# Performance work log

Measured on AMD Instinct MI355X. Metric: run time of the kernel, lower is better.

## Reference

```python
import jax, jax.numpy as jnp
import numpy as np

N_QUBITS = 12
FAST_DEPTH = 4
FAST_DECAY = 0.9
LATENT = 512
BATCH = 2048


def _apply_ry(state, theta, wire):
    # state: (B, 2**n) real; RY is a real rotation. PennyLane default.qubit:
    # wire 0 is the most-significant bit of the state index.
    B = state.shape[0]
    s = state.reshape(B, 1 << wire, 2, -1)
    h = theta * 0.5
    c = jnp.cos(h)[:, None, None]
    sn = jnp.sin(h)[:, None, None]
    s0, s1 = s[:, :, 0], s[:, :, 1]
    out = jnp.stack([c * s0 - sn * s1, sn * s0 + c * s1], axis=2)
    return out.reshape(state.shape)


def _apply_cnot_adjacent(state, wire):
    # CNOT with control=wire, target=wire+1 (nearest-neighbor chain)
    B = state.shape[0]
    s = state.reshape(B, 1 << wire, 2, 2, -1)
    out = jnp.stack([s[:, :, 0], s[:, :, 1, ::-1]], axis=2)
    return out.reshape(state.shape)


def _fwp_circuit(x, fast, n_qubits, n_outputs):
    # x: (B, n_qubits) RY encoding angles; fast: (B, depth, n_qubits)
    B = x.shape[0]
    dim = 1 << n_qubits
    # Hadamard layer on |0...0> -> uniform positive real amplitudes.
    state = jnp.full((B, dim), 2.0 ** (-n_qubits / 2), dtype=x.dtype)
    for w in range(n_qubits):
        state = _apply_ry(state, x[:, w], w)
    for layer in range(fast.shape[1]):
        for w in range(n_qubits - 1):
            state = _apply_cnot_adjacent(state, w)
        for w in range(n_qubits):
            state = _apply_ry(state, fast[:, layer, w], w)
    probs = state * state  # real state -> |amp|^2
    outs = []
    for w in range(n_outputs):
        p = probs.reshape(B, 1 << w, 2, -1)
        outs.append(p[:, :, 0].sum(axis=(1, 2)) - p[:, :, 1].sum(axis=(1, 2)))
    return jnp.stack(outs, axis=1)  # (B, n_outputs) PauliZ expvals


def setup_inputs() -> dict:
    key = jax.random.key(0)
    ks = jax.random.split(key, 6)
    n, depth, latent = N_QUBITS, FAST_DEPTH, LATENT
    return {
        "x_t": jax.random.normal(ks[0], (BATCH, n), jnp.float32),
        "fast_prev": jax.random.normal(ks[1], (BATCH, depth, n), jnp.float32) * 0.1,
        "W_enc": jax.random.normal(ks[2], (latent, n), jnp.float32) / np.sqrt(n).astype(np.float32),
        "b_enc": jnp.zeros((latent,), jnp.float32),
        "W_upd": jax.random.normal(ks[3], (depth * n, latent), jnp.float32) / np.sqrt(latent).astype(np.float32),
        "b_upd": jnp.zeros((depth * n,), jnp.float32),
        "W_ro": jax.random.normal(ks[4], (1, n), jnp.float32) / np.sqrt(n).astype(np.float32),
        "b_ro": jnp.zeros((1,), jnp.float32),
    }


def reference(x_t, fast_prev, W_enc, b_enc, W_upd, b_upd, W_ro, b_ro):
    latent = jnp.tanh(x_t @ W_enc.T + b_enc)
    delta = (latent @ W_upd.T + b_upd).reshape(x_t.shape[0], FAST_DEPTH, N_QUBITS)
    fast_next = FAST_DECAY * fast_prev + delta
    q_out = _fwp_circuit(x_t, fast_next, N_QUBITS, N_QUBITS)  # n_outputs = n_qubits
    y_t = q_out @ W_ro.T + b_ro
    return (y_t, fast_next)
```

## Files before the change

### kernel.cpp

```cpp
#include <hip/hip_runtime.h>

static constexpr int NQ    = 12;
static constexpr int DEPTH = 4;
static constexpr int LAT   = 512;
static constexpr int FAST  = DEPTH * NQ;
static constexpr float DECAY = 0.9f;
static constexpr int P     = 68;

using v2f = __attribute__((ext_vector_type(2))) float;


__device__ __forceinline__ constexpr int G6(int x)  { return (x ^ (x >> 1)) & 63; }
__device__ __forceinline__ constexpr int GINV(int x){ int y = x; y ^= y >> 1; y ^= y >> 2; y ^= y >> 4; return y & 63; }

template<int CTRL>
__device__ __forceinline__ float dppf(float x){
    return __int_as_float(__builtin_amdgcn_mov_dpp(__float_as_int(x), CTRL, 0xF, 0xF, false));
}
template<int B> __device__ __forceinline__ float lexch(float x);
template<> __device__ __forceinline__ float lexch<0>(float x){ return dppf<0xB1>(x); }
template<> __device__ __forceinline__ float lexch<1>(float x){ return dppf<0x4E>(x); }
template<> __device__ __forceinline__ float lexch<2>(float x){ return dppf<0x141>(dppf<0x1B>(x)); }
template<> __device__ __forceinline__ float lexch<3>(float x){ return dppf<0x128>(x); }
template<> __device__ __forceinline__ float lexch<4>(float x){
    return __int_as_float(__builtin_amdgcn_ds_swizzle(__float_as_int(x), 0x401F));
}

template<int B>
__device__ __forceinline__ void lanewire(float (&t)[64], float c, float ss){
    #pragma unroll
    for (int k = 0; k < 64; k++){
        float p = lexch<B>(t[k]);
        t[k] = __builtin_fmaf(c, t[k], ss * p);
    }
}

template<int B>
__device__ __forceinline__ void regwire(float (&t)[64], float c, float s){
    constexpr int M = (B == 0) ? 1 : ((1 << B) | (1 << (B - 1)));
    #pragma unroll
    for (int k = 0; k < 64; k++){
        if (__builtin_parity((unsigned)(k >> B)) == 0){
            float a = t[k], b = t[k ^ M];
            t[k]     = c * a - s * b;
            t[k ^ M] = s * a + c * b;
        }
    }
}

__device__ __forceinline__ void stageW(const float (&t)[64], float* X, int wbase){
    #pragma unroll
    for (int m = 0; m < 16; m++)
        *(float4*)&X[wbase + 4*m] =
            (float4){ t[G6(4*m+0)], t[G6(4*m+1)], t[G6(4*m+2)], t[G6(4*m+3)] };
}

__device__ __forceinline__ void stageR0(float (&t)[64], const float* X, int rs, int rp, int off,
                                        float c0, float ss0){
    #pragma unroll
    for (int m = 0; m < 16; m++){
        int col = (4*m) ^ off;
        float4 a = *(const float4*)&X[rs + col];
        float4 b = *(const float4*)&X[rp + col];
        t[4*m+0] = __builtin_fmaf(c0, a.x, ss0 * b.x);
        t[4*m+1] = __builtin_fmaf(c0, a.y, ss0 * b.y);
        t[4*m+2] = __builtin_fmaf(c0, a.z, ss0 * b.z);
        t[4*m+3] = __builtin_fmaf(c0, a.w, ss0 * b.w);
    }
}

__device__ __forceinline__ void wiresLane(float (&t)[64], const v2f* c, int lane){
    { v2f cs = c[1]; lanewire<4>(t, cs.x, (lane & 16) ? cs.y : -cs.y); }
    { v2f cs = c[2]; lanewire<3>(t, cs.x, (lane &  8) ? cs.y : -cs.y); }
    { v2f cs = c[3]; lanewire<2>(t, cs.x, (lane &  4) ? cs.y : -cs.y); }
    { v2f cs = c[4]; lanewire<1>(t, cs.x, (lane &  2) ? cs.y : -cs.y); }
    { v2f cs = c[5]; lanewire<0>(t, cs.x, (lane &  1) ? cs.y : -cs.y); }
}
__device__ __forceinline__ void wiresReg(float (&t)[64], const v2f* c){
    { v2f cs = c[6];  regwire<5>(t, cs.x, cs.y); }
    { v2f cs = c[7];  regwire<4>(t, cs.x, cs.y); }
    { v2f cs = c[8];  regwire<3>(t, cs.x, cs.y); }
    { v2f cs = c[9];  regwire<2>(t, cs.x, cs.y); }
    { v2f cs = c[10]; regwire<1>(t, cs.x, cs.y); }
    { v2f cs = c[11]; regwire<0>(t, cs.x, cs.y); }
}

__device__ __forceinline__ void init_state(float (&v)[64], const float (&xa)[NQ], int lane) {
    float g0[NQ], g1[NQ];
    #pragma unroll
    for (int w = 0; w < NQ; w++) {
        float hh = 0.5f * xa[w];
        float c = __cosf(hh), s = __sinf(hh);
        g0[w] = (c - s) * 0.70710678118654752f;
        g1[w] = (c + s) * 0.70710678118654752f;
    }
    float L = 1.0f;
    #pragma unroll
    for (int w = 0; w < 6; w++)
        L *= ((lane >> (5 - w)) & 1) ? g1[w] : g0[w];
    v[0] = L;
    #pragma unroll
    for (int w = 6; w < NQ; w++) {
        const int S = 1 << (11 - w);
        #pragma unroll
        for (int r = 0; r < 64; r += 2 * S) {
            v[r + S] = v[r] * g1[w];
            v[r]     = v[r] * g0[w];
        }
    }
}

__global__ __launch_bounds__(64, 1)
void fwp_kernel(const float* __restrict__ x_t,
                const float* __restrict__ fast_prev,
                const float* __restrict__ W_enc,
                const float* __restrict__ b_enc,
                const float* __restrict__ W_upd,
                const float* __restrict__ b_upd,
                const float* __restrict__ W_ro,
                const float* __restrict__ b_ro,
                float* __restrict__ out_y,
                float* __restrict__ out_fast) {
    const int lane = threadIdx.x;
    const int eA   = 2 * blockIdx.x;
    const int eB   = eA + 1;

    __shared__ __align__(16) float XA[64 * P];
    __shared__ __align__(16) float XB[64 * P];
    __shared__ __align__(8)  v2f   csA[FAST], csB[FAST];

    float* latA = XA;
    float* latB = XB;

    float xaA[NQ], xaB[NQ];
    #pragma unroll
    for (int k = 0; k < NQ; k++) {
        xaA[k] = x_t[eA * NQ + k];
        xaB[k] = x_t[eB * NQ + k];
    }

    {
        const float4* we = (const float4*)(W_enc + lane * 8 * NQ);
        float4 be0 = *(const float4*)&b_enc[8 * lane];
        float4 be1 = *(const float4*)&b_enc[8 * lane + 4];
        float be[8] = {be0.x, be0.y, be0.z, be0.w, be1.x, be1.y, be1.z, be1.w};
        float lA[8], lB[8];
        #pragma unroll
        for (int t = 0; t < 8; t++) {
            float4 a0 = we[3 * t], a1 = we[3 * t + 1], a2 = we[3 * t + 2];
            float sA = be[t]
                + a0.x * xaA[0] + a0.y * xaA[1] + a0.z * xaA[2]  + a0.w * xaA[3]
                + a1.x * xaA[4] + a1.y * xaA[5] + a1.z * xaA[6]  + a1.w * xaA[7]
                + a2.x * xaA[8] + a2.y * xaA[9] + a2.z * xaA[10] + a2.w * xaA[11];
            float sB = be[t]
                + a0.x * xaB[0] + a0.y * xaB[1] + a0.z * xaB[2]  + a0.w * xaB[3]
                + a1.x * xaB[4] + a1.y * xaB[5] + a1.z * xaB[6]  + a1.w * xaB[7]
                + a2.x * xaB[8] + a2.y * xaB[9] + a2.z * xaB[10] + a2.w * xaB[11];
            lA[t] = tanhf(sA);
            lB[t] = tanhf(sB);
        }
        *(float4*)&latA[8 * lane]     = (float4){lA[0], lA[1], lA[2], lA[3]};
        *(float4*)&latA[8 * lane + 4] = (float4){lA[4], lA[5], lA[6], lA[7]};
        *(float4*)&latB[8 * lane]     = (float4){lB[0], lB[1], lB[2], lB[3]};
        *(float4*)&latB[8 * lane + 4] = (float4){lB[4], lB[5], lB[6], lB[7]};
    }

    if (lane < FAST) {
        const float4* wr = (const float4*)(W_upd + lane * LAT);
        const float4* la = (const float4*)(latA);
        const float4* lb = (const float4*)(latB);
        float base = b_upd[lane];
        float sA = base, sB = base;
        #pragma unroll 8
        for (int j = 0; j < LAT / 4; j++) {
            float4 w4 = wr[j];
            float4 a4 = la[j];
            float4 b4 = lb[j];
            sA += w4.x * a4.x + w4.y * a4.y + w4.z * a4.z + w4.w * a4.w;
            sB += w4.x * b4.x + w4.y * b4.y + w4.z * b4.z + w4.w * b4.w;
        }
        float angA = DECAY * fast_prev[eA * FAST + lane] + sA;
        float angB = DECAY * fast_prev[eB * FAST + lane] + sB;
        out_fast[eA * FAST + lane] = angA;
        out_fast[eB * FAST + lane] = angB;
        csA[lane] = (v2f){__cosf(0.5f * angA), __sinf(0.5f * angA)};
        csB[lane] = (v2f){__cosf(0.5f * angB), __sinf(0.5f * angB)};
    }

    float tmp[64], tA[64], tB[64];
    init_state(tmp, xaA, lane);
    #pragma unroll
    for (int k = 0; k < 64; k++) tA[k] = tmp[GINV(k)];
    init_state(tmp, xaB, lane);
    #pragma unroll
    for (int k = 0; k < 64; k++) tB[k] = tmp[GINV(k)];

    const int wbase = lane * P;
    const int gl    = (lane ^ (lane >> 1)) & 63;
    const int rs    = gl * P;
    const int rp    = (gl ^ 48) * P;
    const int off   = (lane & 1) * 32;

    #pragma unroll 1
    for (int layer = 0; layer < DEPTH; layer++) {
        const v2f* cA = csA + layer * NQ;
        const v2f* cB = csB + layer * NQ;
        v2f a0 = cA[0], b0 = cB[0];
        float ssA0 = (lane & 32) ? a0.y : -a0.y;
        float ssB0 = (lane & 32) ? b0.y : -b0.y;

        stageW(tA, XA, wbase);
        stageR0(tA, XA, rs, rp, off, a0.x, ssA0);
        stageW(tB, XB, wbase);
        wiresLane(tA, cA, lane);
        stageR0(tB, XB, rs, rp, off, b0.x, ssB0);
        wiresReg(tA, cA);
        wiresLane(tB, cB, lane);
        wiresReg(tB, cB);
    }

    float wro[NQ];
    #pragma unroll
    for (int w = 0; w < NQ; w++) wro[w] = W_ro[w];
    float sl = 0.0f;
    #pragma unroll
    for (int w = 0; w < 6; w++)
        sl += ((lane >> (5 - w)) & 1) ? -wro[w] : wro[w];

    float totA = 0.0f, pwA[6] = {0,0,0,0,0,0};
    float totB = 0.0f, pwB[6] = {0,0,0,0,0,0};
    #pragma unroll
    for (int r = 0; r < 64; r++) {
        float aA = tA[G6(r)], aB = tB[G6(r)];
        float pA = aA * aA;
        float pB = aB * aB;
        totA += pA;  totB += pB;
        pwA[0] += (r & 32) ? -pA : pA;  pwB[0] += (r & 32) ? -pB : pB;
        pwA[1] += (r & 16) ? -pA : pA;  pwB[1] += (r & 16) ? -pB : pB;
        pwA[2] += (r & 8)  ? -pA : pA;  pwB[2] += (r & 8)  ? -pB : pB;
        pwA[3] += (r & 4)  ? -pA : pA;  pwB[3] += (r & 4)  ? -pB : pB;
        pwA[4] += (r & 2)  ? -pA : pA;  pwB[4] += (r & 2)  ? -pB : pB;
        pwA[5] += (r & 1)  ? -pA : pA;  pwB[5] += (r & 1)  ? -pB : pB;
    }
    float yA = sl * totA, yB = sl * totB;
    #pragma unroll
    for (int k = 0; k < 6; k++) {
        yA += wro[6 + k] * pwA[k];
        yB += wro[6 + k] * pwB[k];
    }
    #pragma unroll
    for (int m = 32; m >= 1; m >>= 1) {
        yA += __shfl_xor(yA, m, 64);
        yB += __shfl_xor(yB, m, 64);
    }
    if (lane == 0) {
        float br = b_ro[0];
        out_y[eA] = yA + br;
        out_y[eB] = yB + br;
    }
}

extern "C" void kernel_launch(void* const* d_in, const int* in_sizes, int n_in,
                              void* d_out, int out_size, void* d_ws, size_t ws_size,
                              hipStream_t stream) {
    const float* x_t       = (const float*)d_in[0];
    const float* fast_prev = (const float*)d_in[1];
    const float* W_enc     = (const float*)d_in[2];
    const float* b_enc     = (const float*)d_in[3];
    const float* W_upd     = (const float*)d_in[4];
    const float* b_upd     = (const float*)d_in[5];
    const float* W_ro      = (const float*)d_in[6];
    const float* b_ro      = (const float*)d_in[7];
    float* out = (float*)d_out;

    fwp_kernel<<<1024, 64, 0, stream>>>(x_t, fast_prev, W_enc, b_enc,
                                        W_upd, b_upd, W_ro, b_ro,
                                        out , out + 2048 );
}
```

Baseline: 121.6 us.

## Interleave both batch elements into packed v2f state to use packed FP32 math

Stores the two batch elements' amplitudes interleaved as float2 pairs so rotations run as packed v2f multiply/FMA operations that can map to packed FP32 instructions. The register-pair wires now use plain bit indices instead of a Gray-code-permuted layout, and the shared-memory transpose is merged into one wider buffer with a new permuted read pattern. Cos/sin tables are repacked as paired CC/SS arrays. The trade-off is that lane exchanges still need two DPP moves per pair, and register pressure or bank conflicts may change with the wider rows.

```diff
diff --git a/kernel.cpp b/kernel.cpp
--- a/kernel.cpp
+++ b/kernel.cpp
@@ -5,13 +5,12 @@
 static constexpr int LAT   = 512;
 static constexpr int FAST  = DEPTH * NQ;
 static constexpr float DECAY = 0.9f;
-static constexpr int P     = 68;
+static constexpr int PPF   = 132;
 
 using v2f = __attribute__((ext_vector_type(2))) float;
 
 
 __device__ __forceinline__ constexpr int G6(int x)  { return (x ^ (x >> 1)) & 63; }
-__device__ __forceinline__ constexpr int GINV(int x){ int y = x; y ^= y >> 1; y ^= y >> 2; y ^= y >> 4; return y & 63; }
 
 template<int CTRL>
 __device__ __forceinline__ float dppf(float x){
@@ -25,87 +24,28 @@
 template<> __device__ __forceinline__ float lexch<4>(float x){
     return __int_as_float(__builtin_amdgcn_ds_swizzle(__float_as_int(x), 0x401F));
 }
+template<int B> __device__ __forceinline__ v2f lexch2(v2f v){
+    return (v2f){ lexch<B>(v.x), lexch<B>(v.y) };
+}
 
 template<int B>
-__device__ __forceinline__ void lanewire(float (&t)[64], float c, float ss){
+__device__ __forceinline__ void lanewire2(v2f (&u)[64], v2f cc, v2f ssv){
     #pragma unroll
     for (int k = 0; k < 64; k++){
-        float p = lexch<B>(t[k]);
-        t[k] = __builtin_fmaf(c, t[k], ss * p);
-    }
-}
-
-template<int B>
-__device__ __forceinline__ void regwire(float (&t)[64], float c, float s){
-    constexpr int M = (B == 0) ? 1 : ((1 << B) | (1 << (B - 1)));
-    #pragma unroll
-    for (int k = 0; k < 64; k++){
-        if (__builtin_parity((unsigned)(k >> B)) == 0){
-            float a = t[k], b = t[k ^ M];
-            t[k]     = c * a - s * b;
-            t[k ^ M] = s * a + c * b;
-        }
-    }
-}
-
-__device__ __forceinline__ void stageW(const float (&t)[64], float* X, int wbase){
-    #pragma unroll
-    for (int m = 0; m < 16; m++)
-        *(float4*)&X[wbase + 4*m] =
-            (float4){ t[G6(4*m+0)], t[G6(4*m+1)], t[G6(4*m+2)], t[G6(4*m+3)] };
-}
-
-__device__ __forceinline__ void stageR0(float (&t)[64], const float* X, int rs, int rp, int off,
-                                        float c0, float ss0){
-    #pragma unroll
-    for (int m = 0; m < 16; m++){
-        int col = (4*m) ^ off;
-        float4 a = *(const float4*)&X[rs + col];
-        float4 b = *(const float4*)&X[rp + col];
-        t[4*m+0] = __builtin_fmaf(c0, a.x, ss0 * b.x);
-        t[4*m+1] = __builtin_fmaf(c0, a.y, ss0 * b.y);
-        t[4*m+2] = __builtin_fmaf(c0, a.z, ss0 * b.z);
-        t[4*m+3] = __builtin_fmaf(c0, a.w, ss0 * b.w);
-    }
-}
-
-__device__ __forceinline__ void wiresLane(float (&t)[64], const v2f* c, int lane){
-    { v2f cs = c[1]; lanewire<4>(t, cs.x, (lane & 16) ? cs.y : -cs.y); }
-    { v2f cs = c[2]; lanewire<3>(t, cs.x, (lane &  8) ? cs.y : -cs.y); }
-    { v2f cs = c[3]; lanewire<2>(t, cs.x, (lane &  4) ? cs.y : -cs.y); }
-    { v2f cs = c[4]; lanewire<1>(t, cs.x, (lane &  2) ? cs.y : -cs.y); }
-    { v2f cs = c[5]; lanewire<0>(t, cs.x, (lane &  1) ? cs.y : -cs.y); }
-}
-__device__ __forceinline__ void wiresReg(float (&t)[64], const v2f* c){
-    { v2f cs = c[6];  regwire<5>(t, cs.x, cs.y); }
-    { v2f cs = c[7];  regwire<4>(t, cs.x, cs.y); }
-    { v2f cs = c[8];  regwire<3>(t, cs.x, cs.y); }
-    { v2f cs = c[9];  regwire<2>(t, cs.x, cs.y); }
-    { v2f cs = c[10]; regwire<1>(t, cs.x, cs.y); }
-    { v2f cs = c[11]; regwire<0>(t, cs.x, cs.y); }
-}
-
-__device__ __forceinline__ void init_state(float (&v)[64], const float (&xa)[NQ], int lane) {
-    float g0[NQ], g1[NQ];
-    #pragma unroll
-    for (int w = 0; w < NQ; w++) {
-        float hh = 0.5f * xa[w];
-        float c = __cosf(hh), s = __sinf(hh);
-        g0[w] = (c - s) * 0.70710678118654752f;
-        g1[w] = (c + s) * 0.70710678118654752f;
-    }
-    float L = 1.0f;
-    #pragma unroll
-    for (int w = 0; w < 6; w++)
-        L *= ((lane >> (5 - w)) & 1) ? g1[w] : g0[w];
-    v[0] = L;
-    #pragma unroll
-    for (int w = 6; w < NQ; w++) {
-        const int S = 1 << (11 - w);
-        #pragma unroll
-        for (int r = 0; r < 64; r += 2 * S) {
-            v[r + S] = v[r] * g1[w];
-            v[r]     = v[r] * g0[w];
+        v2f p = lexch2<B>(u[k]);
+        u[k] = cc * u[k] + ssv * p;
+    }
+}
+
+template<int BIT>
+__device__ __forceinline__ void regwire2(v2f (&u)[64], v2f cc, v2f ss){
+    constexpr int M = 1 << BIT;
+    #pragma unroll
+    for (int r = 0; r < 64; r++){
+        if (!(r & M)){
+            v2f a = u[r], b = u[r ^ M];
+            u[r]     = cc * a - ss * b;
+            u[r ^ M] = ss * a + cc * b;
         }
     }
 }
@@ -125,12 +65,11 @@
     const int eA   = 2 * blockIdx.x;
     const int eB   = eA + 1;
 
-    __shared__ __align__(16) float XA[64 * P];
-    __shared__ __align__(16) float XB[64 * P];
-    __shared__ __align__(8)  v2f   csA[FAST], csB[FAST];
-
-    float* latA = XA;
-    float* latB = XB;
+    __shared__ __align__(16) float Xs[64 * PPF];
+    __shared__ __align__(8)  v2f CC[FAST], SS[FAST];
+
+    float* latA = Xs;
+    float* latB = Xs + LAT;
 
     float xaA[NQ], xaB[NQ];
     #pragma unroll
@@ -183,40 +122,93 @@
         float angB = DECAY * fast_prev[eB * FAST + lane] + sB;
         out_fast[eA * FAST + lane] = angA;
         out_fast[eB * FAST + lane] = angB;
-        csA[lane] = (v2f){__cosf(0.5f * angA), __sinf(0.5f * angA)};
-        csB[lane] = (v2f){__cosf(0.5f * angB), __sinf(0.5f * angB)};
-    }
-
-    float tmp[64], tA[64], tB[64];
-    init_state(tmp, xaA, lane);
-    #pragma unroll
-    for (int k = 0; k < 64; k++) tA[k] = tmp[GINV(k)];
-    init_state(tmp, xaB, lane);
-    #pragma unroll
-    for (int k = 0; k < 64; k++) tB[k] = tmp[GINV(k)];
-
-    const int wbase = lane * P;
-    const int gl    = (lane ^ (lane >> 1)) & 63;
-    const int rs    = gl * P;
-    const int rp    = (gl ^ 48) * P;
-    const int off   = (lane & 1) * 32;
+        CC[lane] = (v2f){__cosf(0.5f * angA), __cosf(0.5f * angB)};
+        SS[lane] = (v2f){__sinf(0.5f * angA), __sinf(0.5f * angB)};
+    }
+
+    v2f u[64];
+    {
+        v2f g0[NQ], g1[NQ];
+        #pragma unroll
+        for (int w = 0; w < NQ; w++) {
+            float hA = 0.5f * xaA[w], hB = 0.5f * xaB[w];
+            float cA = __cosf(hA), sA = __sinf(hA);
+            float cB = __cosf(hB), sB = __sinf(hB);
+            const float K = 0.70710678118654752f;
+            g0[w] = (v2f){(cA - sA) * K, (cB - sB) * K};
+            g1[w] = (v2f){(cA + sA) * K, (cB + sB) * K};
+        }
+        v2f L = (v2f){1.0f, 1.0f};
+        #pragma unroll
+        for (int w = 0; w < 6; w++)
+            L *= ((lane >> (5 - w)) & 1) ? g1[w] : g0[w];
+        u[0] = L;
+        #pragma unroll
+        for (int w = 6; w < NQ; w++) {
+            const int S = 1 << (11 - w);
+            #pragma unroll
+            for (int r = 0; r < 64; r += 2 * S) {
+                u[r + S] = u[r] * g1[w];
+                u[r]     = u[r] * g0[w];
+            }
+        }
+    }
+
+    const int g    = G6(lane);
+    const int gp   = g ^ 48;
+    const int off2 = (lane & 1) * 64;
+    const float* s_lo = Xs + g  * PPF + off2;
+    const float* s_hi = Xs + g  * PPF + (off2 ^ 64);
+    const float* p_lo = Xs + gp * PPF + off2;
+    const float* p_hi = Xs + gp * PPF + (off2 ^ 64);
+    float* wrow = Xs + lane * PPF;
 
     #pragma unroll 1
     for (int layer = 0; layer < DEPTH; layer++) {
-        const v2f* cA = csA + layer * NQ;
-        const v2f* cB = csB + layer * NQ;
-        v2f a0 = cA[0], b0 = cB[0];
-        float ssA0 = (lane & 32) ? a0.y : -a0.y;
-        float ssB0 = (lane & 32) ? b0.y : -b0.y;
-
-        stageW(tA, XA, wbase);
-        stageR0(tA, XA, rs, rp, off, a0.x, ssA0);
-        stageW(tB, XB, wbase);
-        wiresLane(tA, cA, lane);
-        stageR0(tB, XB, rs, rp, off, b0.x, ssB0);
-        wiresReg(tA, cA);
-        wiresLane(tB, cB, lane);
-        wiresReg(tB, cB);
+        v2f cc[NQ], ss[NQ];
+        #pragma unroll
+        for (int w = 0; w < NQ; w++) { cc[w] = CC[layer * NQ + w]; ss[w] = SS[layer * NQ + w]; }
+        v2f ss0 = (lane & 32) ? ss[0] : -ss[0];
+
+        #pragma unroll
+        for (int k = 0; k < 32; k++)
+            *(float4*)&wrow[4 * k] =
+                (float4){u[2 * k].x, u[2 * k].y, u[2 * k + 1].x, u[2 * k + 1].y};
+
+        #pragma unroll
+        for (int b = 0; b < 16; b++) {
+            const int q = b ^ (b >> 1);
+            const float* ps = (q < 8) ? s_lo + 8 * q : s_hi + 8 * (q - 8);
+            const float* pq = (q < 8) ? p_lo + 8 * q : p_hi + 8 * (q - 8);
+            float4 sa = *(const float4*)ps, sb = *(const float4*)(ps + 4);
+            float4 pa = *(const float4*)pq, pb = *(const float4*)(pq + 4);
+            v2f w0 = {sa.x, sa.y}, w1 = {sa.z, sa.w}, w2v = {sb.x, sb.y}, w3 = {sb.z, sb.w};
+            v2f p0 = {pa.x, pa.y}, p1 = {pa.z, pa.w}, p2v = {pb.x, pb.y}, p3 = {pb.z, pb.w};
+            if ((b & 1) == 0) {
+                u[4 * b + 0] = cc[0] * w0  + ss0 * p0;
+                u[4 * b + 1] = cc[0] * w1  + ss0 * p1;
+                u[4 * b + 2] = cc[0] * w3  + ss0 * p3;
+                u[4 * b + 3] = cc[0] * w2v + ss0 * p2v;
+            } else {
+                u[4 * b + 0] = cc[0] * w2v + ss0 * p2v;
+                u[4 * b + 1] = cc[0] * w3  + ss0 * p3;
+                u[4 * b + 2] = cc[0] * w1  + ss0 * p1;
+                u[4 * b + 3] = cc[0] * w0  + ss0 * p0;
+            }
+        }
+
+        { v2f sv = (lane & 16) ? ss[1] : -ss[1]; lanewire2<4>(u, cc[1], sv); }
+        { v2f sv = (lane &  8) ? ss[2] : -ss[2]; lanewire2<3>(u, cc[2], sv); }
+        { v2f sv = (lane &  4) ? ss[3] : -ss[3]; lanewire2<2>(u, cc[3], sv); }
+        { v2f sv = (lane &  2) ? ss[4] : -ss[4]; lanewire2<1>(u, cc[4], sv); }
+        { v2f sv = (lane &  1) ? ss[5] : -ss[5]; lanewire2<0>(u, cc[5], sv); }
+
+        regwire2<5>(u, cc[6],  ss[6]);
+        regwire2<4>(u, cc[7],  ss[7]);
+        regwire2<3>(u, cc[8],  ss[8]);
+        regwire2<2>(u, cc[9],  ss[9]);
+        regwire2<1>(u, cc[10], ss[10]);
+        regwire2<0>(u, cc[11], ss[11]);
     }
 
     float wro[NQ];
@@ -227,27 +219,25 @@
     for (int w = 0; w < 6; w++)
         sl += ((lane >> (5 - w)) & 1) ? -wro[w] : wro[w];
 
-    float totA = 0.0f, pwA[6] = {0,0,0,0,0,0};
-    float totB = 0.0f, pwB[6] = {0,0,0,0,0,0};
+    v2f tot = (v2f){0.0f, 0.0f};
+    v2f pw[6];
+    #pragma unroll
+    for (int k = 0; k < 6; k++) pw[k] = (v2f){0.0f, 0.0f};
     #pragma unroll
     for (int r = 0; r < 64; r++) {
-        float aA = tA[G6(r)], aB = tB[G6(r)];
-        float pA = aA * aA;
-        float pB = aB * aB;
-        totA += pA;  totB += pB;
-        pwA[0] += (r & 32) ? -pA : pA;  pwB[0] += (r & 32) ? -pB : pB;
-        pwA[1] += (r & 16) ? -pA : pA;  pwB[1] += (r & 16) ? -pB : pB;
-        pwA[2] += (r & 8)  ? -pA : pA;  pwB[2] += (r & 8)  ? -pB : pB;
-        pwA[3] += (r & 4)  ? -pA : pA;  pwB[3] += (r & 4)  ? -pB : pB;
-        pwA[4] += (r & 2)  ? -pA : pA;  pwB[4] += (r & 2)  ? -pB : pB;
-        pwA[5] += (r & 1)  ? -pA : pA;  pwB[5] += (r & 1)  ? -pB : pB;
-    }
-    float yA = sl * totA, yB = sl * totB;
-    #pragma unroll
-    for (int k = 0; k < 6; k++) {
-        yA += wro[6 + k] * pwA[k];
-        yB += wro[6 + k] * pwB[k];
-    }
+        v2f p = u[r] * u[r];
+        tot += p;
+        pw[0] += (r & 32) ? -p : p;
+        pw[1] += (r & 16) ? -p : p;
+        pw[2] += (r & 8)  ? -p : p;
+        pw[3] += (r & 4)  ? -p : p;
+        pw[4] += (r & 2)  ? -p : p;
+        pw[5] += (r & 1)  ? -p : p;
+    }
+    v2f y2 = (v2f){sl, sl} * tot;
+    #pragma unroll
+    for (int k = 0; k < 6; k++) y2 += (v2f){wro[6 + k], wro[6 + k]} * pw[k];
+    float yA = y2.x, yB = y2.y;
     #pragma unroll
     for (int m = 32; m >= 1; m >>= 1) {
         yA += __shfl_xor(yA, m, 64);
```

After: 117.3 us. 3.5% less time.
